# Kernel optimization log

Measured on AMD Instinct MI355X. Metric: run time of the kernel, lower is better.

## Reference

```python
import jax, jax.numpy as jnp
import numpy as np

SIGMA = 5.0


def setup_inputs() -> dict:
    key = jax.random.key(0)
    ks = jax.random.split(key, 10)
    D, H, K0, K1 = 2048, 2048, 16, 8
    return {
        "inputs": jax.random.normal(ks[0], (1, D), jnp.float32),
        "cluster_center": jax.random.normal(ks[1], (K0, D), jnp.float32),
        "leaf_weight_u": jax.random.normal(ks[2], (K0, D, H), jnp.float32),
        "leaf_bias_u": jax.random.normal(ks[3], (K0, H), jnp.float32),
        "no_leaf_weight_i": jax.random.normal(ks[4], (K1, H), jnp.float32),
        "no_leaf_bias_i": jax.random.normal(ks[5], (K1,), jnp.float32),
        "no_leaf_weight_u": jax.random.normal(ks[6], (K1, H, H), jnp.float32),
        "no_leaf_bias_u": jax.random.normal(ks[7], (K1, H), jnp.float32),
        "root_weight_u": jax.random.normal(ks[8], (H, H), jnp.float32),
        "root_bias_u": jax.random.normal(ks[9], (1, H), jnp.float32),
    }


def reference(inputs, cluster_center, leaf_weight_u, leaf_bias_u,
              no_leaf_weight_i, no_leaf_bias_i, no_leaf_weight_u,
              no_leaf_bias_u, root_weight_u, root_bias_u):
    x = inputs[0]  # (D,)
    # soft assignment to cluster centers: exp(-||x-c||^2/(2*sigma)) / sum(...)
    diff = x[None, :] - cluster_center               # (K0, D)
    sq = jnp.sum(diff * diff, axis=-1)               # (K0,)
    assign = jax.nn.softmax(-sq / (2.0 * SIGMA))     # (K0,)
    # leaf cells: assignment-weighted tanh projections
    value_u = jnp.tanh(jnp.einsum('d,kdh->kh', x, leaf_weight_u) + leaf_bias_u)  # (K0, H)
    c_leaf = assign[:, None] * value_u               # (K0, H)
    # non-leaf gating: softmax over cluster_layer_1 per leaf
    gate_logits = jnp.einsum('kh,jh->kj', c_leaf, no_leaf_weight_i) + no_leaf_bias_i[None, :]  # (K0, K1)
    gate = jax.nn.softmax(gate_logits, axis=1)       # (K0, K1)
    u = jnp.tanh(jnp.einsum('kh,jhg->kjg', c_leaf, no_leaf_weight_u) + no_leaf_bias_u[None, :, :])  # (K0, K1, H)
    c_no_leaf = jnp.sum(gate[:, :, None] * u, axis=0)  # sum over K0 -> (K1, H)
    # root: sum over cluster_layer_1
    root = jnp.tanh(c_no_leaf @ root_weight_u + root_bias_u)  # (K1, H)
    root_c = jnp.sum(root, axis=0, keepdims=True)    # (1, H)
    return (root_c, root_c)
```

## Files before the change

kernel.cpp:

```cpp
#include <hip/hip_runtime.h>
#include <math.h>

#define D   2048
#define H   2048
#define K0  16
#define KJ  8

#define WS_ASSIGN  0
#define WS_GATE    64
#define WS_CLEAF   256
#define WS_PLEAF   33280
#define WS_PNL     557568
#define WS_CNL     2654720
#define WS_PROOT   2671104

__global__ void k_assign(const float* __restrict__ x, const float* __restrict__ cc,
                         float* __restrict__ ws) {
    __shared__ float red[256];
    __shared__ float sq[K0];
    int t = threadIdx.x;
    for (int k = 0; k < K0; ++k) {
        float a = 0.f;
        for (int d = t; d < D; d += 256) {
            float df = x[d] - cc[k * D + d];
            a += df * df;
        }
        red[t] = a; __syncthreads();
        for (int s = 128; s > 0; s >>= 1) {
            if (t < s) red[t] += red[t + s];
            __syncthreads();
        }
        if (t == 0) sq[k] = red[0];
        __syncthreads();
    }
    if (t == 0) {
        float m = -1e30f;
        for (int k = 0; k < K0; ++k) {
            float v = -sq[k] * 0.1f;
            sq[k] = v;
            m = fmaxf(m, v);
        }
        float s = 0.f;
        for (int k = 0; k < K0; ++k) { sq[k] = expf(sq[k] - m); s += sq[k]; }
        float inv = 1.0f / s;
        for (int k = 0; k < K0; ++k) ws[WS_ASSIGN + k] = sq[k] * inv;
    }
}

__global__ void k_leaf_partial(const float* __restrict__ x, const float* __restrict__ W,
                               float* __restrict__ ws) {
    const int k  = blockIdx.x;
    const int h0 = blockIdx.y * 1024;
    const int dc = blockIdx.z;
    const int d0 = dc * 128;
    __shared__ float xs[128];
    int t = threadIdx.x;
    if (t < 128) xs[t] = x[d0 + t];
    __syncthreads();
    int h = h0 + t * 4;
    const float* Wp = W + ((size_t)k * D + d0) * (size_t)H + h;
    float4 acc = make_float4(0.f, 0.f, 0.f, 0.f);
#pragma unroll 8
    for (int dd = 0; dd < 128; ++dd) {
        float4 w = *(const float4*)(Wp + (size_t)dd * H);
        float xv = xs[dd];
        acc.x += xv * w.x; acc.y += xv * w.y; acc.z += xv * w.z; acc.w += xv * w.w;
    }
    *(float4*)(ws + WS_PLEAF + ((size_t)(dc * K0 + k)) * H + h) = acc;
}

__global__ void k_cleaf(const float* __restrict__ lb, float* __restrict__ ws) {
    int idx = blockIdx.x * 256 + threadIdx.x;
    int k = idx >> 11;
    int h = idx & (H - 1);
    float s = 0.f;
#pragma unroll
    for (int dc = 0; dc < 16; ++dc)
        s += ws[WS_PLEAF + ((size_t)(dc * K0 + k) << 11) + h];
    float v = tanhf(s + lb[k * H + h]) * ws[WS_ASSIGN + k];
    ws[WS_CLEAF + k * H + h] = v;
}

__global__ void k_gate(const float* __restrict__ Wi, const float* __restrict__ bi,
                       float* __restrict__ ws) {
    int k = blockIdx.x;
    int t = threadIdx.x;
    const float* cl = ws + WS_CLEAF + k * H;
    float acc[KJ];
#pragma unroll
    for (int j = 0; j < KJ; ++j) acc[j] = 0.f;
    for (int h = t; h < H; h += 256) {
        float c = cl[h];
#pragma unroll
        for (int j = 0; j < KJ; ++j) acc[j] += c * Wi[j * H + h];
    }
    __shared__ float red[KJ][256];
#pragma unroll
    for (int j = 0; j < KJ; ++j) red[j][t] = acc[j];
    __syncthreads();
    for (int s = 128; s > 0; s >>= 1) {
        if (t < s) {
#pragma unroll
            for (int j = 0; j < KJ; ++j) red[j][t] += red[j][t + s];
        }
        __syncthreads();
    }
    if (t == 0) {
        float l[KJ], m = -1e30f;
#pragma unroll
        for (int j = 0; j < KJ; ++j) { l[j] = red[j][0] + bi[j]; m = fmaxf(m, l[j]); }
        float s = 0.f;
#pragma unroll
        for (int j = 0; j < KJ; ++j) { l[j] = expf(l[j] - m); s += l[j]; }
        float inv = 1.0f / s;
#pragma unroll
        for (int j = 0; j < KJ; ++j) ws[WS_GATE + k * KJ + j] = l[j] * inv;
    }
}

__global__ void k_nl_partial(const float* __restrict__ Wn, float* __restrict__ ws) {
    const int j  = blockIdx.x;
    const int g0 = blockIdx.y * 512;
    const int hc = blockIdx.z;
    const int h0 = hc * 256;
    __shared__ float cls[K0][256];
    int t = threadIdx.x;
    for (int i = t; i < K0 * 256; i += 256) {
        int k = i >> 8, hh = i & 255;
        cls[k][hh] = ws[WS_CLEAF + k * H + h0 + hh];
    }
    __syncthreads();
    int g = g0 + t * 2;
    const float* Wp = Wn + ((size_t)j * H + h0) * (size_t)H + g;
    float2 acc[K0];
#pragma unroll
    for (int k = 0; k < K0; ++k) { acc[k].x = 0.f; acc[k].y = 0.f; }
#pragma unroll 4
    for (int hh = 0; hh < 256; ++hh) {
        float2 w = *(const float2*)(Wp + (size_t)hh * H);
#pragma unroll
        for (int k = 0; k < K0; ++k) {
            float c = cls[k][hh];
            acc[k].x += c * w.x; acc[k].y += c * w.y;
        }
    }
#pragma unroll
    for (int k = 0; k < K0; ++k)
        *(float2*)(ws + WS_PNL + ((size_t)((hc * KJ + j) * K0 + k) << 11) + g) = acc[k];
}

__global__ void k_cnl(const float* __restrict__ nb, float* __restrict__ ws) {
    int idx = blockIdx.x * 256 + threadIdx.x;
    int j = idx >> 11;
    int g = idx & (H - 1);
    float out = 0.f;
#pragma unroll
    for (int k = 0; k < K0; ++k) {
        float s = 0.f;
#pragma unroll
        for (int hc = 0; hc < 8; ++hc)
            s += ws[WS_PNL + ((size_t)((hc * KJ + j) * K0 + k) << 11) + g];
        float u = tanhf(s + nb[j * H + g]);
        out += ws[WS_GATE + k * KJ + j] * u;
    }
    ws[WS_CNL + j * H + g] = out;
}

__global__ void k_root_partial(const float* __restrict__ Wr, float* __restrict__ ws) {
    const int g2t = blockIdx.x;
    const int gc  = blockIdx.y;
    const int g0  = gc * 64;
    __shared__ float cns[KJ][64];
    int t = threadIdx.x;
    for (int i = t; i < KJ * 64; i += 256) {
        int j = i >> 6, gg = i & 63;
        cns[j][gg] = ws[WS_CNL + j * H + g0 + gg];
    }
    __syncthreads();
    int g2 = g2t * 512 + t * 2;
    float2 acc[KJ];
#pragma unroll
    for (int j = 0; j < KJ; ++j) { acc[j].x = 0.f; acc[j].y = 0.f; }
#pragma unroll 4
    for (int gg = 0; gg < 64; ++gg) {
        float2 w = *(const float2*)(Wr + (size_t)(g0 + gg) * H + g2);
#pragma unroll
        for (int j = 0; j < KJ; ++j) {
            float c = cns[j][gg];
            acc[j].x += c * w.x; acc[j].y += c * w.y;
        }
    }
#pragma unroll
    for (int j = 0; j < KJ; ++j)
        *(float2*)(ws + WS_PROOT + ((size_t)(gc * KJ + j) << 11) + g2) = acc[j];
}

__global__ void k_final(const float* __restrict__ rb, float* __restrict__ ws,
                        float* __restrict__ out) {
    int g2 = blockIdx.x * 256 + threadIdx.x;
    float tot = 0.f;
#pragma unroll
    for (int j = 0; j < KJ; ++j) {
        float s = 0.f;
#pragma unroll
        for (int gc = 0; gc < 32; ++gc)
            s += ws[WS_PROOT + ((size_t)(gc * KJ + j) << 11) + g2];
        tot += tanhf(s + rb[g2]);
    }
    out[g2] = tot;
    out[2048 + g2] = tot;
}

extern "C" void kernel_launch(void* const* d_in, const int* in_sizes, int n_in,
                              void* d_out, int out_size, void* d_ws, size_t ws_size,
                              hipStream_t stream) {
    const float* x  = (const float*)d_in[0];
    const float* cc = (const float*)d_in[1];
    const float* lw = (const float*)d_in[2];
    const float* lb = (const float*)d_in[3];
    const float* wi = (const float*)d_in[4];
    const float* bi = (const float*)d_in[5];
    const float* wn = (const float*)d_in[6];
    const float* nb = (const float*)d_in[7];
    const float* wr = (const float*)d_in[8];
    const float* rb = (const float*)d_in[9];
    float* out = (float*)d_out;
    float* ws  = (float*)d_ws;

    k_assign      <<<1, 256, 0, stream>>>(x, cc, ws);
    k_leaf_partial<<<dim3(16, 2, 16), 256, 0, stream>>>(x, lw, ws);
    k_cleaf       <<<128, 256, 0, stream>>>(lb, ws);
    k_gate        <<<16, 256, 0, stream>>>(wi, bi, ws);
    k_nl_partial  <<<dim3(8, 4, 8), 256, 0, stream>>>(wn, ws);
    k_cnl         <<<64, 256, 0, stream>>>(nb, ws);
    k_root_partial<<<dim3(4, 32), 256, 0, stream>>>(wr, ws);
    k_final       <<<8, 256, 0, stream>>>(rb, ws, out);
}
```

Baseline: 595.9 us.

## Skip leaf clusters with negligible soft assignment and deepen split-K partitioning

Leaf-projection blocks and the c_leaf combine now exit early for any cluster whose softmax assignment is below 1e-7. Because tanh is bounded, those clusters contribute almost nothing, so most of the large leaf weight tensor need not be read. The leaf and non-leaf partial GEMVs split their reduction dimension into twice as many chunks for more parallelism, which doubles the partial-sum traffic in the workspace. The assignment kernel now uses one wave per cluster with shuffle reductions, and the root tanh is moved into its own parallel kernel before the final sum.

```diff
diff --git a/kernel.cpp b/kernel.cpp
--- a/kernel.cpp
+++ b/kernel.cpp
@@ -6,78 +6,83 @@
 #define K0  16
 #define KJ  8
 
-#define WS_ASSIGN  0
-#define WS_GATE    64
-#define WS_CLEAF   256
-#define WS_PLEAF   33280
-#define WS_PNL     557568
-#define WS_CNL     2654720
-#define WS_PROOT   2671104
+#define SKIP_THR 1e-7f
+
+#define WS_ASSIGN 0
+#define WS_GATE   64
+#define WS_CLEAF  256
+#define WS_PLEAF  33024
+#define WS_PNL    1081600
+#define WS_CNL    5275904
+#define WS_PROOT  5292288
+#define WS_TMP    5816576
 
 __global__ void k_assign(const float* __restrict__ x, const float* __restrict__ cc,
                          float* __restrict__ ws) {
-    __shared__ float red[256];
+    int t = threadIdx.x, w = t >> 6, l = t & 63;
+    const float4* c4 = (const float4*)(cc + w * D);
+    const float4* x4 = (const float4*)x;
+    float a = 0.f;
+#pragma unroll
+    for (int i = 0; i < 8; ++i) {
+        float4 xv = x4[l + i * 64];
+        float4 cv = c4[l + i * 64];
+        float dx = xv.x - cv.x, dy = xv.y - cv.y;
+        float dz = xv.z - cv.z, dw = xv.w - cv.w;
+        a += dx * dx + dy * dy + dz * dz + dw * dw;
+    }
+#pragma unroll
+    for (int off = 32; off > 0; off >>= 1) a += __shfl_down(a, off);
     __shared__ float sq[K0];
-    int t = threadIdx.x;
-    for (int k = 0; k < K0; ++k) {
-        float a = 0.f;
-        for (int d = t; d < D; d += 256) {
-            float df = x[d] - cc[k * D + d];
-            a += df * df;
-        }
-        red[t] = a; __syncthreads();
-        for (int s = 128; s > 0; s >>= 1) {
-            if (t < s) red[t] += red[t + s];
-            __syncthreads();
-        }
-        if (t == 0) sq[k] = red[0];
-        __syncthreads();
-    }
+    if (l == 0) sq[w] = a;
+    __syncthreads();
     if (t == 0) {
-        float m = -1e30f;
-        for (int k = 0; k < K0; ++k) {
-            float v = -sq[k] * 0.1f;
-            sq[k] = v;
-            m = fmaxf(m, v);
-        }
-        float s = 0.f;
-        for (int k = 0; k < K0; ++k) { sq[k] = expf(sq[k] - m); s += sq[k]; }
+        float v[K0], m = -1e30f;
+#pragma unroll
+        for (int k = 0; k < K0; ++k) { v[k] = -sq[k] * 0.1f; m = fmaxf(m, v[k]); }
+        float s = 0.f;
+#pragma unroll
+        for (int k = 0; k < K0; ++k) { v[k] = expf(v[k] - m); s += v[k]; }
         float inv = 1.0f / s;
-        for (int k = 0; k < K0; ++k) ws[WS_ASSIGN + k] = sq[k] * inv;
+#pragma unroll
+        for (int k = 0; k < K0; ++k) ws[WS_ASSIGN + k] = v[k] * inv;
     }
 }
 
 __global__ void k_leaf_partial(const float* __restrict__ x, const float* __restrict__ W,
                                float* __restrict__ ws) {
-    const int k  = blockIdx.x;
+    const int k = blockIdx.x;
+    if (ws[WS_ASSIGN + k] < SKIP_THR) return;
     const int h0 = blockIdx.y * 1024;
-    const int dc = blockIdx.z;
-    const int d0 = dc * 128;
-    __shared__ float xs[128];
-    int t = threadIdx.x;
-    if (t < 128) xs[t] = x[d0 + t];
+    const int d0 = blockIdx.z * 64;
+    __shared__ float xs[64];
+    int t = threadIdx.x;
+    if (t < 64) xs[t] = x[d0 + t];
     __syncthreads();
     int h = h0 + t * 4;
     const float* Wp = W + ((size_t)k * D + d0) * (size_t)H + h;
     float4 acc = make_float4(0.f, 0.f, 0.f, 0.f);
-#pragma unroll 8
-    for (int dd = 0; dd < 128; ++dd) {
+#pragma unroll 16
+    for (int dd = 0; dd < 64; ++dd) {
         float4 w = *(const float4*)(Wp + (size_t)dd * H);
         float xv = xs[dd];
         acc.x += xv * w.x; acc.y += xv * w.y; acc.z += xv * w.z; acc.w += xv * w.w;
     }
-    *(float4*)(ws + WS_PLEAF + ((size_t)(dc * K0 + k)) * H + h) = acc;
+    *(float4*)(ws + WS_PLEAF + ((size_t)(blockIdx.z * K0 + k) << 11) + h) = acc;
 }
 
 __global__ void k_cleaf(const float* __restrict__ lb, float* __restrict__ ws) {
     int idx = blockIdx.x * 256 + threadIdx.x;
-    int k = idx >> 11;
-    int h = idx & (H - 1);
-    float s = 0.f;
-#pragma unroll
-    for (int dc = 0; dc < 16; ++dc)
-        s += ws[WS_PLEAF + ((size_t)(dc * K0 + k) << 11) + h];
-    float v = tanhf(s + lb[k * H + h]) * ws[WS_ASSIGN + k];
+    int k = idx >> 11, h = idx & (H - 1);
+    float az = ws[WS_ASSIGN + k];
+    float v = 0.f;
+    if (az >= SKIP_THR) {
+        float s = 0.f;
+#pragma unroll
+        for (int dc = 0; dc < 32; ++dc)
+            s += ws[WS_PLEAF + ((size_t)(dc * K0 + k) << 11) + h];
+        v = tanhf(s + lb[k * H + h]) * az;
+    }
     ws[WS_CLEAF + k * H + h] = v;
 }
 
@@ -121,12 +126,11 @@
 __global__ void k_nl_partial(const float* __restrict__ Wn, float* __restrict__ ws) {
     const int j  = blockIdx.x;
     const int g0 = blockIdx.y * 512;
-    const int hc = blockIdx.z;
-    const int h0 = hc * 256;
-    __shared__ float cls[K0][256];
-    int t = threadIdx.x;
-    for (int i = t; i < K0 * 256; i += 256) {
-        int k = i >> 8, hh = i & 255;
+    const int h0 = blockIdx.z * 128;
+    __shared__ float cls[K0][128];
+    int t = threadIdx.x;
+    for (int i = t; i < K0 * 128; i += 256) {
+        int k = i >> 7, hh = i & 127;
         cls[k][hh] = ws[WS_CLEAF + k * H + h0 + hh];
     }
     __syncthreads();
@@ -135,8 +139,8 @@
     float2 acc[K0];
 #pragma unroll
     for (int k = 0; k < K0; ++k) { acc[k].x = 0.f; acc[k].y = 0.f; }
-#pragma unroll 4
-    for (int hh = 0; hh < 256; ++hh) {
+#pragma unroll 8
+    for (int hh = 0; hh < 128; ++hh) {
         float2 w = *(const float2*)(Wp + (size_t)hh * H);
 #pragma unroll
         for (int k = 0; k < K0; ++k) {
@@ -146,30 +150,28 @@
     }
 #pragma unroll
     for (int k = 0; k < K0; ++k)
-        *(float2*)(ws + WS_PNL + ((size_t)((hc * KJ + j) * K0 + k) << 11) + g) = acc[k];
+        *(float2*)(ws + WS_PNL + ((size_t)((blockIdx.z * KJ + j) * K0 + k) << 11) + g) = acc[k];
 }
 
 __global__ void k_cnl(const float* __restrict__ nb, float* __restrict__ ws) {
-    int idx = blockIdx.x * 256 + threadIdx.x;
-    int j = idx >> 11;
-    int g = idx & (H - 1);
+    int idx = blockIdx.x * 128 + threadIdx.x;
+    int j = idx >> 11, g = idx & (H - 1);
+    float bias = nb[j * H + g];
     float out = 0.f;
 #pragma unroll
     for (int k = 0; k < K0; ++k) {
         float s = 0.f;
 #pragma unroll
-        for (int hc = 0; hc < 8; ++hc)
+        for (int hc = 0; hc < 16; ++hc)
             s += ws[WS_PNL + ((size_t)((hc * KJ + j) * K0 + k) << 11) + g];
-        float u = tanhf(s + nb[j * H + g]);
-        out += ws[WS_GATE + k * KJ + j] * u;
+        out += ws[WS_GATE + k * KJ + j] * tanhf(s + bias);
     }
     ws[WS_CNL + j * H + g] = out;
 }
 
 __global__ void k_root_partial(const float* __restrict__ Wr, float* __restrict__ ws) {
     const int g2t = blockIdx.x;
-    const int gc  = blockIdx.y;
-    const int g0  = gc * 64;
+    const int g0  = blockIdx.y * 64;
     __shared__ float cns[KJ][64];
     int t = threadIdx.x;
     for (int i = t; i < KJ * 64; i += 256) {
@@ -181,7 +183,7 @@
     float2 acc[KJ];
 #pragma unroll
     for (int j = 0; j < KJ; ++j) { acc[j].x = 0.f; acc[j].y = 0.f; }
-#pragma unroll 4
+#pragma unroll 8
     for (int gg = 0; gg < 64; ++gg) {
         float2 w = *(const float2*)(Wr + (size_t)(g0 + gg) * H + g2);
 #pragma unroll
@@ -192,23 +194,26 @@
     }
 #pragma unroll
     for (int j = 0; j < KJ; ++j)
-        *(float2*)(ws + WS_PROOT + ((size_t)(gc * KJ + j) << 11) + g2) = acc[j];
-}
-
-__global__ void k_final(const float* __restrict__ rb, float* __restrict__ ws,
-                        float* __restrict__ out) {
+        *(float2*)(ws + WS_PROOT + ((size_t)(blockIdx.y * KJ + j) << 11) + g2) = acc[j];
+}
+
+__global__ void k_root_tanh(const float* __restrict__ rb, float* __restrict__ ws) {
+    int j  = blockIdx.x;
+    int g2 = blockIdx.y * 256 + threadIdx.x;
+    float s = 0.f;
+#pragma unroll
+    for (int gc = 0; gc < 32; ++gc)
+        s += ws[WS_PROOT + ((size_t)(gc * KJ + j) << 11) + g2];
+    ws[WS_TMP + j * H + g2] = tanhf(s + rb[g2]);
+}
+
+__global__ void k_final(float* __restrict__ ws, float* __restrict__ out) {
     int g2 = blockIdx.x * 256 + threadIdx.x;
     float tot = 0.f;
 #pragma unroll
-    for (int j = 0; j < KJ; ++j) {
-        float s = 0.f;
-#pragma unroll
-        for (int gc = 0; gc < 32; ++gc)
-            s += ws[WS_PROOT + ((size_t)(gc * KJ + j) << 11) + g2];
-        tot += tanhf(s + rb[g2]);
-    }
+    for (int j = 0; j < KJ; ++j) tot += ws[WS_TMP + j * H + g2];
     out[g2] = tot;
-    out[2048 + g2] = tot;
+    out[H + g2] = tot;
 }
 
 extern "C" void kernel_launch(void* const* d_in, const int* in_sizes, int n_in,
@@ -227,12 +232,13 @@
     float* out = (float*)d_out;
     float* ws  = (float*)d_ws;
 
-    k_assign      <<<1, 256, 0, stream>>>(x, cc, ws);
-    k_leaf_partial<<<dim3(16, 2, 16), 256, 0, stream>>>(x, lw, ws);
+    k_assign      <<<1, 1024, 0, stream>>>(x, cc, ws);
+    k_leaf_partial<<<dim3(16, 2, 32), 256, 0, stream>>>(x, lw, ws);
     k_cleaf       <<<128, 256, 0, stream>>>(lb, ws);
     k_gate        <<<16, 256, 0, stream>>>(wi, bi, ws);
-    k_nl_partial  <<<dim3(8, 4, 8), 256, 0, stream>>>(wn, ws);
-    k_cnl         <<<64, 256, 0, stream>>>(nb, ws);
+    k_nl_partial  <<<dim3(8, 4, 16), 256, 0, stream>>>(wn, ws);
+    k_cnl         <<<128, 128, 0, stream>>>(nb, ws);
     k_root_partial<<<dim3(4, 32), 256, 0, stream>>>(wr, ws);
-    k_final       <<<8, 256, 0, stream>>>(rb, ws, out);
-}
+    k_root_tanh   <<<dim3(8, 8), 256, 0, stream>>>(rb, ws);
+    k_final       <<<8, 256, 0, stream>>>(ws, out);
+}
```

After: 500.9 us. 15.9% less time.
